# Kernel tuning notes

Measured on AMD Instinct MI355X. Metric: run time of the kernel, lower is better.

Reference implementation:

```python
import jax, jax.numpy as jnp
import numpy as np

INV_SQRT2 = 0.7071067811865476


def _quadrature_ops(d):
    # truncated harmonic-oscillator ladder operator: a[n, n+1] = sqrt(n+1)
    a = jnp.diag(jnp.sqrt(jnp.arange(1, d, dtype=jnp.float32)), k=1)
    X0 = (a + a.T) * INV_SQRT2
    P0 = (a - a.T) * INV_SQRT2  # real-valued stand-in for the momentum quadrature
    I = jnp.eye(d, dtype=jnp.float32)
    return I, X0, P0


def setup_inputs() -> dict:
    key = jax.random.key(0)
    ks = jax.random.split(key, 6)
    D, d, w, K = 512, 32, 8, 4
    return {
        "mps_params": jax.random.normal(ks[0], (D, d, D), dtype=jnp.float32),
        "theta": jax.random.normal(ks[1], (1,), dtype=jnp.float32),
        "env_L": jax.random.normal(ks[2], (K, D, w, D), dtype=jnp.float32) * 0.1,
        "env_R": jax.random.normal(ks[3], (K, D, w, D), dtype=jnp.float32) * 0.1,
        "coeffs": jax.random.normal(ks[4], (K, w, w, 5), dtype=jnp.float32),
        "prefactors": jax.random.normal(ks[5], (K,), dtype=jnp.float32),
    }


def reference(mps_params, theta, env_L, env_R, coeffs, prefactors):
    A = mps_params  # [D(left), d(phys), D(right)]
    d = A.shape[1]
    K = prefactors.shape[0]

    # norm_fn: psi.H @ psi for a single-tensor MPS is sum(A^2)
    An = A / jnp.sqrt(jnp.sum(A * A))

    # _get_XandP: quadrature rotation from basis params
    I, X0, P0 = _quadrature_ops(d)
    c, s = jnp.cos(theta[0]), jnp.sin(theta[0])
    X = c * X0 + s * P0
    P = -s * X0 + c * P0

    # dynamic MPO cores: W_k[i,j] = sum_c coeffs[k,i,j,c] * ops[c]
    ops = jnp.stack([I, X, P, X @ X, P @ P])  # [5, d, d]
    W = jnp.einsum('kijc,cab->kijab', coeffs, ops)  # [K, w, w, d, d]

    out = jnp.zeros((), dtype=A.dtype)
    for k in range(K):  # fixed small loop over Hamiltonian constituents
        # T: [L, w, p, r]
        T = jnp.einsum('Lwl,lpr->Lwpr', env_L[k], An)
        # apply MPO core: [L, v, P, r]
        T = jnp.einsum('wvPp,Lwpr->LvPr', W[k], T)
        # close with right env: [L, P, R]
        T = jnp.einsum('LvPr,Rvr->LPR', T, env_R[k])
        out = out + prefactors[k] * jnp.einsum('LPR,LPR->', An, T)
    return out
```

## Files before the change

kernel.cpp:

```cpp
#include <hip/hip_runtime.h>


typedef __attribute__((ext_vector_type(8))) _Float16 f16x8;
typedef __attribute__((ext_vector_type(4))) float f32x4;

#define RPS 280

__device__ __forceinline__ unsigned short f2h(float f) {
    _Float16 h = (_Float16)f;
    return *(unsigned short*)&h;
}

__device__ __forceinline__ void gload16(const void* g, void* l) {
    __builtin_amdgcn_global_load_lds(
        (const __attribute__((address_space(1))) void*)g,
        (__attribute__((address_space(3))) void*)l, 16, 0, 0);
}

struct GArg {
    const unsigned short* A;
    const unsigned short* B;
    unsigned short* C;
    int kshift;
    long long kextra;
};

__device__ __forceinline__ void stage_tile(
    const GArg& g, int srow0, int col0, int kt0,
    short* dstA, short* dstB, int tid)
{
    #pragma unroll
    for (int q = 0; q < 4; ++q) {
        const int c = q * 512 + tid;
        const int r = c >> 3;
        const int gs = (c & 7) ^ (r & 7);
        const int gr = srow0 + r;
        const size_t aoff = (size_t)gr * 512 + (size_t)((unsigned)gr >> g.kshift) * g.kextra;
        gload16(g.A + aoff + kt0 + gs * 8, dstA + c * 8);
        gload16(g.B + (size_t)(col0 + r) * 512 + kt0 + gs * 8, dstB + c * 8);
    }
}

__global__ __launch_bounds__(512, 1) void gemm_dual_mega(int K, int NPB, GArg g0, GArg g1)
{
    __shared__ short lds[74496];
    const GArg g = blockIdx.z ? g1 : g0;
    const int tid = threadIdx.x;
    const int wid = tid >> 6, lane = tid & 63;
    const int wm = wid >> 2, wn = wid & 3;
    const int lrow = lane & 15, lgrp = lane >> 4;
    const int sx = lrow & 7;
    const int gsw0 = (lgrp ^ sx) * 8, gsw1 = ((lgrp + 4) ^ sx) * 8;

    const int xcd = blockIdx.x & 7, loc = blockIdx.x >> 3;
    const int col0 = (xcd * 8 + loc) * 256;
    const int row_base = blockIdx.y * NPB * 256;

    short* A0 = lds;          short* B0 = lds + 16384;
    short* A1 = lds + 32768;  short* B1 = lds + 49152;
    short* repk = lds + 65536;

    const int NT = (K >> 6) * NPB;

    f32x4 acc[8][4] = {};

    stage_tile(g, row_base, col0, 0, A0, B0, tid);
    stage_tile(g, row_base, col0, 64, A1, B1, tid);
    asm volatile("s_waitcnt vmcnt(8)" ::: "memory");
    __builtin_amdgcn_s_barrier();
    __builtin_amdgcn_sched_barrier(0);

    for (int it = 0; it < NT; ++it) {
        const short* cA = (it & 1) ? A1 : A0;
        const short* cB = (it & 1) ? B1 : B0;
        short* wA = (it & 1) ? A1 : A0;
        short* wB = (it & 1) ? B1 : B0;

        f16x8 bfr[4][2], afr[4][2];
        #pragma unroll
        for (int j = 0; j < 4; ++j) {
            const int R = wn * 64 + j * 16 + lrow;
            bfr[j][0] = *(const f16x8*)&cB[R * 64 + gsw0];
            bfr[j][1] = *(const f16x8*)&cB[R * 64 + gsw1];
        }
        #pragma unroll
        for (int i = 0; i < 4; ++i) {
            const int R = wm * 128 + i * 16 + lrow;
            afr[i][0] = *(const f16x8*)&cA[R * 64 + gsw0];
            afr[i][1] = *(const f16x8*)&cA[R * 64 + gsw1];
        }
        __builtin_amdgcn_s_setprio(1);
        #pragma unroll
        for (int i = 0; i < 4; ++i)
            #pragma unroll
            for (int j = 0; j < 4; ++j) {
                acc[i][j] = __builtin_amdgcn_mfma_f32_16x16x32_f16(afr[i][0], bfr[j][0], acc[i][j], 0, 0, 0);
                acc[i][j] = __builtin_amdgcn_mfma_f32_16x16x32_f16(afr[i][1], bfr[j][1], acc[i][j], 0, 0, 0);
            }
        __builtin_amdgcn_s_setprio(0);
        #pragma unroll
        for (int i = 0; i < 4; ++i) {
            const int R = wm * 128 + (i + 4) * 16 + lrow;
            afr[i][0] = *(const f16x8*)&cA[R * 64 + gsw0];
            afr[i][1] = *(const f16x8*)&cA[R * 64 + gsw1];
        }
        asm volatile("s_waitcnt lgkmcnt(0)" ::: "memory");
        __builtin_amdgcn_sched_barrier(0);
        __builtin_amdgcn_s_barrier();
        __builtin_amdgcn_sched_barrier(0);
        if (it + 2 < NT) {
            const int it2 = it + 2;
            stage_tile(g, row_base + (it2 >> 3) * 256, col0, (it2 & 7) * 64, wA, wB, tid);
        }
        __builtin_amdgcn_s_setprio(1);
        #pragma unroll
        for (int i = 0; i < 4; ++i)
            #pragma unroll
            for (int j = 0; j < 4; ++j) {
                acc[i + 4][j] = __builtin_amdgcn_mfma_f32_16x16x32_f16(afr[i][0], bfr[j][0], acc[i + 4][j], 0, 0, 0);
                acc[i + 4][j] = __builtin_amdgcn_mfma_f32_16x16x32_f16(afr[i][1], bfr[j][1], acc[i + 4][j], 0, 0, 0);
            }
        __builtin_amdgcn_s_setprio(0);
        __builtin_amdgcn_sched_barrier(0);
        if (it + 2 < NT) {
            if ((it & 7) == 0 && it != 0)
                asm volatile("s_waitcnt vmcnt(24)" ::: "memory");
            else
                asm volatile("s_waitcnt vmcnt(8)" ::: "memory");
        } else {
            asm volatile("s_waitcnt vmcnt(0)" ::: "memory");
        }
        __builtin_amdgcn_sched_barrier(0);
        __builtin_amdgcn_s_barrier();
        __builtin_amdgcn_sched_barrier(0);

        if ((it & 7) == 7) {
            const int row0 = row_base + (it >> 3) * 256;
            const int orow = lgrp * 4, ocol = lrow;
            #pragma unroll
            for (int c8 = 0; c8 < 8; ++c8) {
                if (wm == (c8 >> 2)) {
                    const int ib = (c8 & 3) * 2;
                    #pragma unroll
                    for (int di = 0; di < 2; ++di)
                        #pragma unroll
                        for (int j = 0; j < 4; ++j)
                            #pragma unroll
                            for (int q = 0; q < 4; ++q)
                                repk[(di * 16 + orow + q) * RPS + wn * 64 + j * 16 + ocol] =
                                    (short)f2h(acc[ib + di][j][q]);
                }
                asm volatile("s_waitcnt lgkmcnt(0)" ::: "memory");
                __builtin_amdgcn_s_barrier();
                #pragma unroll
                for (int s2 = 0; s2 < 2; ++s2) {
                    const int idx = s2 * 512 + tid;
                    const int rr = idx >> 5, cc = idx & 31;
                    *(int4*)(g.C + (size_t)(row0 + c8 * 32 + rr) * 16384 + col0 + cc * 8) =
                        *(const int4*)&repk[rr * RPS + cc * 8];
                }
                asm volatile("s_waitcnt lgkmcnt(0)" ::: "memory");
                __builtin_amdgcn_s_barrier();
            }
            #pragma unroll
            for (int i = 0; i < 8; ++i)
                #pragma unroll
                for (int j = 0; j < 4; ++j)
                    acc[i][j] = (f32x4){0.f, 0.f, 0.f, 0.f};
        }
    }
}

__global__ __launch_bounds__(512, 1) void gemm_g4w(
    const unsigned short* __restrict__ T1, const unsigned short* __restrict__ Yp,
    const float* __restrict__ W2p, float* __restrict__ dacc,
    int Lt8, int zkShift, int BKC)
{
    __shared__ short sh[16384];
    const int tid = threadIdx.x;
    const int wid = tid >> 6, lane = tid & 63;
    const int kidx = blockIdx.x >> zkShift;
    const int kz = (blockIdx.x - (kidx << zkShift)) * BKC;
    const int wm = wid >> 2, wn = wid & 3;
    const int lrow = lane & 15, lgrp = lane >> 4;
    const int rdoff = lrow * 32 + ((lgrp ^ ((lrow >> 1) & 3)) * 8);

    const size_t T1k = (size_t)kidx * Lt8 * 16384;
    const size_t Yk = (size_t)kidx * 4096;

    f32x4 acc[8][4] = {};

    for (int k0 = 0; k0 < BKC; k0 += 32) {
        const int kk = kz + k0;
        const int lt = kk >> 9, rbase = kk & 511;
        #pragma unroll
        for (int q = 0; q < 2; ++q) {
            const int c = q * 512 + tid;
            const int row = c >> 2;
            const int gs = (c & 3) ^ ((row >> 1) & 3);
            const int hi = row >> 5, lo = row & 31;
            gload16(T1 + T1k + (size_t)(lt * 8 + hi) * 16384 + lo * 512 + rbase + gs * 8,
                    sh + c * 8);
            gload16(Yp + Yk + (size_t)(lt * 32 + lo) * 16384 + hi * 512 + rbase + gs * 8,
                    sh + 8192 + c * 8);
        }
        __syncthreads();
        f16x8 a[8], b[4];
        #pragma unroll
        for (int j = 0; j < 4; ++j)
            b[j] = *(const f16x8*)&sh[8192 + (wn * 64 + j * 16) * 32 + rdoff];
        #pragma unroll
        for (int i = 0; i < 8; ++i)
            a[i] = *(const f16x8*)&sh[(wm * 128 + i * 16) * 32 + rdoff];
        #pragma unroll
        for (int i = 0; i < 8; ++i)
            #pragma unroll
            for (int j = 0; j < 4; ++j)
                acc[i][j] = __builtin_amdgcn_mfma_f32_16x16x32_f16(a[i], b[j], acc[i][j], 0, 0, 0);
        __syncthreads();
    }

    const int orow = lgrp * 4, ocol = lrow;
    const float* Wk = W2p + ((size_t)kidx << 16);
    float s = 0.f;
    #pragma unroll
    for (int j = 0; j < 4; ++j) {
        const int n = wn * 64 + j * 16 + ocol;
        const float* wrow = Wk + (size_t)n * 256 + wm * 128 + orow;
        #pragma unroll
        for (int i = 0; i < 8; ++i) {
            float4 wv = *(const float4*)(wrow + i * 16);
            s += wv.x * acc[i][j][0] + wv.y * acc[i][j][1]
               + wv.z * acc[i][j][2] + wv.w * acc[i][j][3];
        }
    }
    __syncthreads();
    float* red = (float*)sh;
    red[tid] = s;
    __syncthreads();
    for (int st = 256; st > 0; st >>= 1) {
        if (tid < st) red[tid] += red[tid + st];
        __syncthreads();
    }
    if (tid == 0) atomicAdd(dacc, red[0]);
}

__global__ __launch_bounds__(256) void cast_sumsq(
    const float* __restrict__ in, unsigned short* __restrict__ out,
    long long n4, float* __restrict__ sumsq)
{
    float p = 0.f;
    for (long long i = (long long)blockIdx.x * blockDim.x + threadIdx.x; i < n4;
         i += (long long)gridDim.x * blockDim.x) {
        float4 v = ((const float4*)in)[i];
        p += v.x * v.x + v.y * v.y + v.z * v.z + v.w * v.w;
        union { unsigned short s[4]; uint2 d; } o;
        o.s[0] = f2h(v.x); o.s[1] = f2h(v.y); o.s[2] = f2h(v.z); o.s[3] = f2h(v.w);
        ((uint2*)out)[i] = o.d;
    }
    __shared__ float sh[256];
    sh[threadIdx.x] = p;
    __syncthreads();
    for (int s = 128; s > 0; s >>= 1) {
        if (threadIdx.x < s) sh[threadIdx.x] += sh[threadIdx.x + s];
        __syncthreads();
    }
    if (threadIdx.x == 0) atomicAdd(sumsq, sh[0]);
}

__global__ void cast_kernel(const float* __restrict__ in, unsigned short* __restrict__ out,
                            long long n4)
{
    for (long long i = (long long)blockIdx.x * blockDim.x + threadIdx.x; i < n4;
         i += (long long)gridDim.x * blockDim.x) {
        float4 v = ((const float4*)in)[i];
        union { unsigned short s[4]; uint2 d; } o;
        o.s[0] = f2h(v.x); o.s[1] = f2h(v.y); o.s[2] = f2h(v.z); o.s[3] = f2h(v.w);
        ((uint2*)out)[i] = o.d;
    }
}

__global__ void transpose_cast(const float* __restrict__ in, unsigned short* __restrict__ out,
                               int R, int C, long long in_stride, long long out_stride)
{
    __shared__ float tile[32][33];
    in += (long long)blockIdx.z * in_stride;
    out += (long long)blockIdx.z * out_stride;
    int c0 = blockIdx.x * 32, r0 = blockIdx.y * 32;
    int tx = threadIdx.x, ty = threadIdx.y;
    #pragma unroll
    for (int i = 0; i < 4; ++i)
        tile[ty + i * 8][tx] = in[(size_t)(r0 + ty + i * 8) * C + c0 + tx];
    __syncthreads();
    #pragma unroll
    for (int i = 0; i < 4; ++i)
        out[(size_t)(c0 + ty + i * 8) * R + r0 + tx] = f2h(tile[tx][ty + i * 8]);
}

__global__ void build_ops(const float* __restrict__ theta, float* __restrict__ ops)
{
    __shared__ float X[32][32], Pm[32][32];
    int i = threadIdx.y, j = threadIdx.x;
    float c = cosf(theta[0]), s = sinf(theta[0]);
    float aij = (j == i + 1) ? sqrtf((float)j) : 0.f;
    float aji = (i == j + 1) ? sqrtf((float)i) : 0.f;
    const float inv = 0.70710678118654752440f;
    float x0 = (aij + aji) * inv;
    float p0 = (aij - aji) * inv;
    X[i][j] = c * x0 + s * p0;
    Pm[i][j] = -s * x0 + c * p0;
    __syncthreads();
    float xx = 0.f, pp = 0.f;
    #pragma unroll
    for (int m = 0; m < 32; ++m) {
        xx += X[i][m] * X[m][j];
        pp += Pm[i][m] * Pm[m][j];
    }
    ops[0 * 1024 + i * 32 + j] = (i == j) ? 1.f : 0.f;
    ops[1 * 1024 + i * 32 + j] = X[i][j];
    ops[2 * 1024 + i * 32 + j] = Pm[i][j];
    ops[3 * 1024 + i * 32 + j] = xx;
    ops[4 * 1024 + i * 32 + j] = pp;
}

__global__ void build_w(const float* __restrict__ coeffs, const float* __restrict__ ops,
                        const float* __restrict__ pref, float* __restrict__ W2)
{
    int b = blockIdx.x;
    int k = b >> 6, w = (b >> 3) & 7, v = b & 7;
    int P = threadIdx.y, p = threadIdx.x;
    const float* cf = coeffs + ((k * 8 + w) * 8 + v) * 5;
    float acc = 0.f;
    #pragma unroll
    for (int c = 0; c < 5; ++c) acc += cf[c] * ops[c * 1024 + P * 32 + p];
    W2[(size_t)k * 65536 + (v * 32 + P) * 256 + (w * 32 + p)] = acc * pref[k];
}

__global__ void finalize_kernel(const float* __restrict__ dacc, const float* __restrict__ sumsq,
                                float* __restrict__ out)
{
    if (threadIdx.x == 0) out[0] = dacc[0] / sumsq[0];
}

extern "C" void kernel_launch(void* const* d_in, const int* in_sizes, int n_in,
                              void* d_out, int out_size, void* d_ws, size_t ws_size,
                              hipStream_t stream)
{
    const float* A      = (const float*)d_in[0];
    const float* theta  = (const float*)d_in[1];
    const float* envL   = (const float*)d_in[2];
    const float* envR   = (const float*)d_in[3];
    const float* coeffs = (const float*)d_in[4];
    const float* pref   = (const float*)d_in[5];
    float* out = (float*)d_out;

    char* ws = (char*)d_ws;
    float* sumsq = (float*)ws;
    float* dacc  = (float*)(ws + 4);
    float* ops   = (float*)(ws + 64);
    float* W2    = (float*)(ws + (32 << 10));
    unsigned short* envLh  = (unsigned short*)(ws + (4ull << 20));
    unsigned short* Ah     = (unsigned short*)(ws + (21ull << 20));
    unsigned short* Ath    = (unsigned short*)(ws + (38ull << 20));
    unsigned short* envRth = (unsigned short*)(ws + (55ull << 20));
    const size_t big0 = 72ull << 20;

    int Lt = 512;
    while (Lt > 16) {
        size_t need = big0 + 2ull * (size_t)Lt * (1ull << 20);
        if (need <= ws_size) break;
        Lt >>= 1;
    }
    unsigned short* T1 = (unsigned short*)(ws + big0);
    unsigned short* Yp = T1 + (size_t)Lt * 524288;

    const int Lt8 = Lt * 8;
    const int kshiftA = __builtin_ctz(Lt8);
    const long long kextraA = 2097152LL - (long long)Lt8 * 512;
    const int NPB = Lt / 16;
    const int KT = Lt * 512;
    const int BKC = 512;
    const int zk = KT / BKC;
    const int zkShift = __builtin_ctz(zk);

    hipMemsetAsync(ws, 0, 64, stream);

    cast_sumsq<<<1024, 256, 0, stream>>>(A, Ah, 2097152LL, sumsq);
    build_ops<<<1, dim3(32, 32), 0, stream>>>(theta, ops);
    build_w<<<256, dim3(32, 32), 0, stream>>>(coeffs, ops, pref, W2);
    cast_kernel<<<2048, 256, 0, stream>>>(envL, envLh, 2097152LL);
    transpose_cast<<<dim3(512, 16, 1), dim3(32, 8), 0, stream>>>(A, Ath, 512, 16384, 0, 0);
    transpose_cast<<<dim3(128, 16, 4), dim3(32, 8), 0, stream>>>(envR, envRth, 512, 4096,
                                                                 2097152LL, 2097152LL);

    const int ntiles = 512 / Lt;
    for (int t = 0; t < ntiles; ++t) {
        GArg g0, g1;
        g0.A = envLh + (size_t)t * Lt8 * 512; g0.B = Ath; g0.C = T1;
        g0.kshift = kshiftA; g0.kextra = kextraA;
        g1.A = Ah + (size_t)t * Lt * 16384; g1.B = envRth; g1.C = Yp;
        g1.kshift = 30; g1.kextra = 0;
        gemm_dual_mega<<<dim3(64, 2, 2), 512, 0, stream>>>(512, NPB, g0, g1);
        gemm_g4w<<<dim3(4 * zk), 512, 0, stream>>>(T1, Yp, W2, dacc, Lt8, zkShift, BKC);
    }
    finalize_kernel<<<1, 64, 0, stream>>>(dacc, sumsq, out);
}
```

Measured before the change: 1.027 ms.

## Fuse preprocessing kernels, shrink L tile to 64, simplify vmcnt waits

```diff
diff --git a/kernel.cpp b/kernel.cpp
--- a/kernel.cpp
+++ b/kernel.cpp
@@ -122,14 +122,8 @@
             }
         __builtin_amdgcn_s_setprio(0);
         __builtin_amdgcn_sched_barrier(0);
-        if (it + 2 < NT) {
-            if ((it & 7) == 0 && it != 0)
-                asm volatile("s_waitcnt vmcnt(24)" ::: "memory");
-            else
-                asm volatile("s_waitcnt vmcnt(8)" ::: "memory");
-        } else {
-            asm volatile("s_waitcnt vmcnt(0)" ::: "memory");
-        }
+        if (it + 2 < NT) asm volatile("s_waitcnt vmcnt(8)" ::: "memory");
+        else             asm volatile("s_waitcnt vmcnt(0)" ::: "memory");
         __builtin_amdgcn_sched_barrier(0);
         __builtin_amdgcn_s_barrier();
         __builtin_amdgcn_sched_barrier(0);
@@ -245,56 +239,63 @@
     if (tid == 0) atomicAdd(dacc, red[0]);
 }
 
-__global__ __launch_bounds__(256) void cast_sumsq(
-    const float* __restrict__ in, unsigned short* __restrict__ out,
-    long long n4, float* __restrict__ sumsq)
-{
+__global__ void a_prep(const float* __restrict__ in, unsigned short* __restrict__ Ah,
+                       unsigned short* __restrict__ Ath, float* __restrict__ sumsq)
+{
+    __shared__ float tile[32][33];
+    const int c0 = blockIdx.x * 32, r0 = blockIdx.y * 32;
+    const int tx = threadIdx.x, ty = threadIdx.y;
     float p = 0.f;
-    for (long long i = (long long)blockIdx.x * blockDim.x + threadIdx.x; i < n4;
-         i += (long long)gridDim.x * blockDim.x) {
-        float4 v = ((const float4*)in)[i];
-        p += v.x * v.x + v.y * v.y + v.z * v.z + v.w * v.w;
+    #pragma unroll
+    for (int i = 0; i < 4; ++i) {
+        const float v = in[(size_t)(r0 + ty + i * 8) * 16384 + c0 + tx];
+        tile[ty + i * 8][tx] = v;
+        p += v * v;
+        Ah[(size_t)(r0 + ty + i * 8) * 16384 + c0 + tx] = f2h(v);
+    }
+    __syncthreads();
+    #pragma unroll
+    for (int i = 0; i < 4; ++i)
+        Ath[(size_t)(c0 + ty + i * 8) * 512 + r0 + tx] = f2h(tile[tx][ty + i * 8]);
+    __shared__ float sh[256];
+    sh[ty * 32 + tx] = p;
+    __syncthreads();
+    const int tid = ty * 32 + tx;
+    for (int s = 128; s > 0; s >>= 1) {
+        if (tid < s) sh[tid] += sh[tid + s];
+        __syncthreads();
+    }
+    if (tid == 0) atomicAdd(sumsq, sh[0]);
+}
+
+__global__ void env_prep(const float* __restrict__ envL, const float* __restrict__ envR,
+                         unsigned short* __restrict__ envLh, unsigned short* __restrict__ envRth)
+{
+    const int z = blockIdx.z;
+    const int tx = threadIdx.x, ty = threadIdx.y;
+    if (z < 4) {
+        __shared__ float tile[32][33];
+        const float* in = envR + (size_t)z * 2097152;
+        unsigned short* out = envRth + (size_t)z * 2097152;
+        const int c0 = blockIdx.x * 32, r0 = blockIdx.y * 32;
+        #pragma unroll
+        for (int i = 0; i < 4; ++i)
+            tile[ty + i * 8][tx] = in[(size_t)(r0 + ty + i * 8) * 4096 + c0 + tx];
+        __syncthreads();
+        #pragma unroll
+        for (int i = 0; i < 4; ++i)
+            out[(size_t)(c0 + ty + i * 8) * 512 + r0 + tx] = f2h(tile[tx][ty + i * 8]);
+    } else {
+        const int k = z - 4;
+        const float4* in = (const float4*)(envL + (size_t)k * 2097152);
+        uint2* out = (uint2*)(envLh + (size_t)k * 2097152);
+        const int flat = blockIdx.y * 128 + blockIdx.x;
+        const int i = flat * 256 + ty * 32 + tx;
+        const float4 v = in[i];
         union { unsigned short s[4]; uint2 d; } o;
         o.s[0] = f2h(v.x); o.s[1] = f2h(v.y); o.s[2] = f2h(v.z); o.s[3] = f2h(v.w);
-        ((uint2*)out)[i] = o.d;
-    }
-    __shared__ float sh[256];
-    sh[threadIdx.x] = p;
-    __syncthreads();
-    for (int s = 128; s > 0; s >>= 1) {
-        if (threadIdx.x < s) sh[threadIdx.x] += sh[threadIdx.x + s];
-        __syncthreads();
-    }
-    if (threadIdx.x == 0) atomicAdd(sumsq, sh[0]);
-}
-
-__global__ void cast_kernel(const float* __restrict__ in, unsigned short* __restrict__ out,
-                            long long n4)
-{
-    for (long long i = (long long)blockIdx.x * blockDim.x + threadIdx.x; i < n4;
-         i += (long long)gridDim.x * blockDim.x) {
-        float4 v = ((const float4*)in)[i];
-        union { unsigned short s[4]; uint2 d; } o;
-        o.s[0] = f2h(v.x); o.s[1] = f2h(v.y); o.s[2] = f2h(v.z); o.s[3] = f2h(v.w);
-        ((uint2*)out)[i] = o.d;
-    }
-}
-
-__global__ void transpose_cast(const float* __restrict__ in, unsigned short* __restrict__ out,
-                               int R, int C, long long in_stride, long long out_stride)
-{
-    __shared__ float tile[32][33];
-    in += (long long)blockIdx.z * in_stride;
-    out += (long long)blockIdx.z * out_stride;
-    int c0 = blockIdx.x * 32, r0 = blockIdx.y * 32;
-    int tx = threadIdx.x, ty = threadIdx.y;
-    #pragma unroll
-    for (int i = 0; i < 4; ++i)
-        tile[ty + i * 8][tx] = in[(size_t)(r0 + ty + i * 8) * C + c0 + tx];
-    __syncthreads();
-    #pragma unroll
-    for (int i = 0; i < 4; ++i)
-        out[(size_t)(c0 + ty + i * 8) * R + r0 + tx] = f2h(tile[tx][ty + i * 8]);
+        out[i] = o.d;
+    }
 }
 
 __global__ void build_ops(const float* __restrict__ theta, float* __restrict__ ops)
@@ -365,7 +366,7 @@
     unsigned short* envRth = (unsigned short*)(ws + (55ull << 20));
     const size_t big0 = 72ull << 20;
 
-    int Lt = 512;
+    int Lt = 64;
     while (Lt > 16) {
         size_t need = big0 + 2ull * (size_t)Lt * (1ull << 20);
         if (need <= ws_size) break;
@@ -385,13 +386,10 @@
 
     hipMemsetAsync(ws, 0, 64, stream);
 
-    cast_sumsq<<<1024, 256, 0, stream>>>(A, Ah, 2097152LL, sumsq);
+    a_prep<<<dim3(512, 16), dim3(32, 8), 0, stream>>>(A, Ah, Ath, sumsq);
+    env_prep<<<dim3(128, 16, 8), dim3(32, 8), 0, stream>>>(envL, envR, envLh, envRth);
     build_ops<<<1, dim3(32, 32), 0, stream>>>(theta, ops);
     build_w<<<256, dim3(32, 32), 0, stream>>>(coeffs, ops, pref, W2);
-    cast_kernel<<<2048, 256, 0, stream>>>(envL, envLh, 2097152LL);
-    transpose_cast<<<dim3(512, 16, 1), dim3(32, 8), 0, stream>>>(A, Ath, 512, 16384, 0, 0);
-    transpose_cast<<<dim3(128, 16, 4), dim3(32, 8), 0, stream>>>(envR, envRth, 512, 4096,
-                                                                 2097152LL, 2097152LL);
 
     const int ntiles = 512 / Lt;
     for (int t = 0; t < ntiles; ++t) {
```

Result: slower. 1.076 ms (+4.7%).
